# Optimization experiments

Measured on AMD Instinct MI355X. Metric: run time of the kernel, lower is better.

The kernel has to match this reference:

```python
import jax, jax.numpy as jnp
import numpy as np

HEADS = 4
DIM_HEAD = 32
DIM = 128
HIDDEN = HEADS * DIM_HEAD  # 128


def setup_inputs() -> dict:
    key = jax.random.key(0)
    k1, k2, k3 = jax.random.split(key, 3)
    B, C, H, W = 16, DIM, 128, 128
    x = jax.random.normal(k1, (B, C, H, W), dtype=jnp.float32)
    # 1x1 convs are pointwise channel mixes: weight [out_ch, in_ch]
    w_qkv = jax.random.normal(k2, (3 * HIDDEN, C), dtype=jnp.float32) * 0.05
    w_out = jax.random.normal(k3, (DIM, HIDDEN), dtype=jnp.float32) * 0.05
    b_out = jnp.zeros((DIM,), dtype=jnp.float32)
    return {"x": x, "w_qkv": w_qkv, "w_out": w_out, "b_out": b_out}


def reference(x, w_qkv, w_out, b_out):
    b, c, H, W = x.shape
    n = H * W
    scale = DIM_HEAD ** -0.5
    # to_qkv: 1x1 conv == channel GEMM -> [b, 3*hidden, n], then split (tf.split axis=1)
    qkv = jnp.einsum('oc,bchw->bohw', w_qkv, x).reshape(b, 3, HEADS, DIM_HEAD, n)
    q, k, v = qkv[:, 0], qkv[:, 1], qkv[:, 2]  # each [b, h, d, n]
    q = q * scale
    k = jax.nn.softmax(k, axis=-1)  # softmax over spatial tokens n
    context = jnp.einsum('bhdn,bhen->bhde', k, v)   # [b, h, d, e], small d x e
    out = jnp.einsum('bhde,bhdn->bhen', context, q)  # [b, h, e, n]
    out = out.reshape(b, HIDDEN, H, W)
    # to_out: 1x1 conv with bias
    return jnp.einsum('oc,bchw->bohw', w_out, out) + b_out[None, :, None, None]
```

## Files before the change

### kernel.cpp

```cpp
#include <hip/hip_runtime.h>
#include <cmath>

#define NBATCH 16
#define NCH    128
#define NPIX   16384
#define NSLOT  32

#define WS_S_OFF 0
#define WS_A_OFF (NBATCH * NSLOT * 128)
#define WS_TOT_FLOATS (WS_A_OFF + NBATCH * NSLOT * 4096)
#define WS_MBF_BYTE ((size_t)WS_TOT_FLOATS * 4)

typedef __bf16 bf16x8 __attribute__((ext_vector_type(8)));
typedef __bf16 bf16x4 __attribute__((ext_vector_type(4)));
typedef __bf16 bf16x2 __attribute__((ext_vector_type(2)));
typedef float  f32x4  __attribute__((ext_vector_type(4)));

#define MFMA16(a, b, c) __builtin_amdgcn_mfma_f32_16x16x32_bf16((a), (b), (c), 0, 0, 0)

__device__ __forceinline__ void barrier_lds() {
    asm volatile("s_waitcnt lgkmcnt(0)\n\ts_barrier" ::: "memory");
}

__global__ __launch_bounds__(256, 2) void k1_partials(const float* __restrict__ x,
                                                      const float* __restrict__ w_qkv,
                                                      float* __restrict__ ws)
{
    const int b = blockIdx.y;
    const int g = blockIdx.x;
    const int t = threadIdx.x;
    const int w = t >> 6;
    const int l = t & 63;
    const int lm = l & 15;
    const int q  = l >> 4;

    __shared__ __align__(16) __bf16 Xs[64][136];
    __shared__ __align__(16) __bf16 Ee[4][32][20][2];
    __shared__ __align__(16) __bf16 Vv[4][32][20][2];

    const float* wkv = w_qkv + 128 * NCH;
    bf16x8 wfrag[4][4];
#pragma unroll
    for (int rt = 0; rt < 4; ++rt) {
        const int row = (rt < 2) ? (w * 32 + rt * 16 + lm)
                                 : (128 + w * 32 + (rt - 2) * 16 + lm);
#pragma unroll
        for (int ks = 0; ks < 4; ++ks) {
            const float* src = wkv + row * NCH + ks * 32 + q * 8;
            float4 p0 = *(const float4*)src;
            float4 p1 = *(const float4*)(src + 4);
            bf16x8 f;
            f[0] = (__bf16)p0.x; f[1] = (__bf16)p0.y; f[2] = (__bf16)p0.z; f[3] = (__bf16)p0.w;
            f[4] = (__bf16)p1.x; f[5] = (__bf16)p1.y; f[6] = (__bf16)p1.z; f[7] = (__bf16)p1.w;
            wfrag[rt][ks] = f;
        }
    }

    f32x4 a_acc[2][2];
#pragma unroll
    for (int dt = 0; dt < 2; ++dt)
#pragma unroll
        for (int et = 0; et < 2; ++et) a_acc[dt][et] = (f32x4)0.f;
    float s8[8];
#pragma unroll
    for (int j = 0; j < 8; ++j) s8[j] = 0.f;

    float fx[8][4];
    const float* xbase = x + (size_t)(b * NCH + w * 32) * NPIX + l;

    {
        const int n0 = g * 64;
#pragma unroll
        for (int rq = 0; rq < 8; ++rq) {
            const float* xb = xbase + (size_t)(rq * 4) * NPIX + n0;
            fx[rq][0] = xb[0];
            fx[rq][1] = xb[NPIX];
            fx[rq][2] = xb[2 * NPIX];
            fx[rq][3] = xb[3 * NPIX];
        }
    }

    for (int ci = 0; ci < 8; ++ci) {
#pragma unroll
        for (int rq = 0; rq < 8; ++rq) {
            bf16x4 pk;
            pk[0] = (__bf16)fx[rq][0]; pk[1] = (__bf16)fx[rq][1];
            pk[2] = (__bf16)fx[rq][2]; pk[3] = (__bf16)fx[rq][3];
            *(bf16x4*)&Xs[l][w * 32 + rq * 4] = pk;
        }
        if (ci < 7) {
            const int n0 = (g + (ci + 1) * 32) * 64;
#pragma unroll
            for (int rq = 0; rq < 8; ++rq) {
                const float* xb = xbase + (size_t)(rq * 4) * NPIX + n0;
                fx[rq][0] = xb[0];
                fx[rq][1] = xb[NPIX];
                fx[rq][2] = xb[2 * NPIX];
                fx[rq][3] = xb[3 * NPIX];
            }
        }
        barrier_lds();

        f32x4 acc[4][4];
#pragma unroll
        for (int rt = 0; rt < 4; ++rt)
#pragma unroll
            for (int ct = 0; ct < 4; ++ct) acc[rt][ct] = (f32x4)0.f;

#pragma unroll
        for (int ks = 0; ks < 4; ++ks) {
            bf16x8 bf[4];
#pragma unroll
            for (int ct = 0; ct < 4; ++ct)
                bf[ct] = *(const bf16x8*)&Xs[ct * 16 + lm][ks * 32 + q * 8];
#pragma unroll
            for (int rt = 0; rt < 4; ++rt)
#pragma unroll
                for (int ct = 0; ct < 4; ++ct)
                    acc[rt][ct] = MFMA16(wfrag[rt][ks], bf[ct], acc[rt][ct]);
        }

#pragma unroll
        for (int hf = 0; hf < 2; ++hf) {
#pragma unroll
            for (int rt = 0; rt < 2; ++rt) {
                f32x4 v0 = acc[rt][hf * 2 + 0];
                f32x4 v1 = acc[rt][hf * 2 + 1];
#pragma unroll
                for (int r = 0; r < 4; ++r) {
                    float e0 = __expf(v0[r]);
                    float e1 = __expf(v1[r]);
                    s8[rt * 4 + r] += e0 + e1;
                    bf16x2 pw; pw[0] = (__bf16)e0; pw[1] = (__bf16)e1;
                    *(bf16x2*)&Ee[w][rt * 16 + q * 4 + r][lm][0] = pw;
                }
            }
#pragma unroll
            for (int rt = 0; rt < 2; ++rt) {
                f32x4 v0 = acc[rt + 2][hf * 2 + 0];
                f32x4 v1 = acc[rt + 2][hf * 2 + 1];
#pragma unroll
                for (int r = 0; r < 4; ++r) {
                    bf16x2 pw; pw[0] = (__bf16)v0[r]; pw[1] = (__bf16)v1[r];
                    *(bf16x2*)&Vv[w][rt * 16 + q * 4 + r][lm][0] = pw;
                }
            }
            {
                bf16x8 ea[2], vb[2];
#pragma unroll
                for (int dt = 0; dt < 2; ++dt)
                    ea[dt] = *(const bf16x8*)&Ee[w][dt * 16 + lm][q * 4][0];
#pragma unroll
                for (int et = 0; et < 2; ++et)
                    vb[et] = *(const bf16x8*)&Vv[w][et * 16 + lm][q * 4][0];
#pragma unroll
                for (int dt = 0; dt < 2; ++dt)
#pragma unroll
                    for (int et = 0; et < 2; ++et)
                        a_acc[dt][et] = MFMA16(ea[dt], vb[et], a_acc[dt][et]);
            }
        }
        barrier_lds();
    }

#pragma unroll
    for (int j = 0; j < 8; ++j) {
        float v = s8[j];
        v += __shfl_xor(v, 1);
        v += __shfl_xor(v, 2);
        v += __shfl_xor(v, 4);
        v += __shfl_xor(v, 8);
        s8[j] = v;
    }
    if (lm == 0) {
        float* Sp = ws + WS_S_OFF + (size_t)(b * NSLOT + g) * 128;
#pragma unroll
        for (int rt2 = 0; rt2 < 2; ++rt2)
#pragma unroll
            for (int r = 0; r < 4; ++r)
                Sp[w * 32 + rt2 * 16 + q * 4 + r] = s8[rt2 * 4 + r];
    }
    {
        float* Ab = ws + WS_A_OFF + (size_t)((b * NSLOT + g) * 4 + w) * 1024;
#pragma unroll
        for (int dt = 0; dt < 2; ++dt)
#pragma unroll
            for (int et = 0; et < 2; ++et)
#pragma unroll
                for (int r = 0; r < 4; ++r)
                    Ab[(dt * 16 + q * 4 + r) * 32 + et * 16 + lm] = a_acc[dt][et][r];
    }
}

__global__ __launch_bounds__(256) void k2_mprime(const float* __restrict__ w_qkv,
                                                 const float* __restrict__ w_out,
                                                 const float* __restrict__ ws,
                                                 __bf16* __restrict__ Mbf)
{
    const int b  = blockIdx.x;
    const int o0 = blockIdx.y * 32;
    const int t  = threadIdx.x;

    __shared__ float ctx[4][32][32];
    __shared__ float Ts[32][128];
    __shared__ float Wqs[32][128];
    __shared__ float Ss[128];

    if (t < 128) {
        float s = 0.f;
#pragma unroll
        for (int r = 0; r < NSLOT; ++r)
            s += ws[WS_S_OFF + (size_t)(b * NSLOT + r) * 128 + t];
        Ss[t] = s;
    }
    __syncthreads();

    for (int i = t; i < 4096; i += 256) {
        float a = 0.f;
#pragma unroll
        for (int r = 0; r < NSLOT; ++r)
            a += ws[WS_A_OFF + (size_t)(b * NSLOT + r) * 4096 + i];
        const int hh = i >> 10, d = (i >> 5) & 31, e = i & 31;
        ctx[hh][d][e] = a / Ss[hh * 32 + d];
    }
    __syncthreads();

    {
        const int oo  = t >> 3;
        const int o   = o0 + oo;
        const int hd0 = (t & 7) * 16;
        const int hh  = hd0 >> 5;
        const int db  = hd0 & 31;
        float wo[32];
#pragma unroll
        for (int e4 = 0; e4 < 32; e4 += 4)
            *(float4*)&wo[e4] = *(const float4*)&w_out[o * NCH + hh * 32 + e4];
#pragma unroll
        for (int k = 0; k < 16; ++k) {
            const int d = db + k;
            float s = 0.f;
#pragma unroll
            for (int e = 0; e < 32; ++e) s = fmaf(wo[e], ctx[hh][d][e], s);
            Ts[oo][hd0 + k] = s;
        }
    }
    __syncthreads();

    float macc[16];
#pragma unroll
    for (int ii = 0; ii < 16; ++ii) macc[ii] = 0.f;

    for (int slab = 0; slab < 4; ++slab) {
        for (int i = t; i < 32 * 128; i += 256)
            Wqs[i >> 7][i & 127] = w_qkv[(size_t)(slab * 32 + (i >> 7)) * NCH + (i & 127)];
        __syncthreads();
#pragma unroll
        for (int ii = 0; ii < 16; ++ii) {
            const int i  = t + ii * 256;
            const int oo = i >> 7;
            const int c  = i & 127;
            float s = macc[ii];
#pragma unroll
            for (int k = 0; k < 32; ++k)
                s = fmaf(Ts[oo][slab * 32 + k], Wqs[k][c], s);
            macc[ii] = s;
        }
        __syncthreads();
    }

    const float scale = 0.17677669529663687f;
#pragma unroll
    for (int ii = 0; ii < 16; ++ii) {
        const int i  = t + ii * 256;
        const int oo = i >> 7;
        const int c  = i & 127;
        Mbf[(size_t)(b * NCH + o0 + oo) * NCH + c] = (__bf16)(macc[ii] * scale);
    }
}

__global__ __launch_bounds__(256, 4) void k3_out(const float* __restrict__ x,
                                                 const float* __restrict__ bias,
                                                 const __bf16* __restrict__ Mbf,
                                                 float* __restrict__ y)
{
    const int b  = blockIdx.y;
    const int n0 = blockIdx.x * 64;
    const int t  = threadIdx.x;
    const int w  = t >> 6, l = t & 63;
    const int lm = l & 15, q = l >> 4;

    __shared__ __align__(16) __bf16 Xs[64][136];

    const __bf16* Mb = Mbf + (size_t)b * NCH * NCH;
    bf16x8 mfrag[2][4];
#pragma unroll
    for (int rt = 0; rt < 2; ++rt)
#pragma unroll
        for (int ks = 0; ks < 4; ++ks)
            mfrag[rt][ks] = *(const bf16x8*)&Mb[(size_t)(w * 32 + rt * 16 + lm) * NCH + ks * 32 + q * 8];

#pragma unroll
    for (int rq = 0; rq < 8; ++rq) {
        const int r0 = w * 32 + rq * 4;
        const float* xb = x + (size_t)(b * NCH + r0) * NPIX + n0 + l;
        float f0 = xb[0], f1 = xb[NPIX], f2 = xb[2 * NPIX], f3 = xb[3 * NPIX];
        bf16x4 pk;
        pk[0] = (__bf16)f0; pk[1] = (__bf16)f1; pk[2] = (__bf16)f2; pk[3] = (__bf16)f3;
        *(bf16x4*)&Xs[l][r0] = pk;
    }
    __syncthreads();

    f32x4 acc[2][4];
#pragma unroll
    for (int rt = 0; rt < 2; ++rt)
#pragma unroll
        for (int ct = 0; ct < 4; ++ct) acc[rt][ct] = (f32x4)0.f;

#pragma unroll
    for (int ks = 0; ks < 4; ++ks) {
        bf16x8 bf[4];
#pragma unroll
        for (int ct = 0; ct < 4; ++ct)
            bf[ct] = *(const bf16x8*)&Xs[ct * 16 + lm][ks * 32 + q * 8];
#pragma unroll
        for (int rt = 0; rt < 2; ++rt)
#pragma unroll
            for (int ct = 0; ct < 4; ++ct)
                acc[rt][ct] = MFMA16(mfrag[rt][ks], bf[ct], acc[rt][ct]);
    }

#pragma unroll
    for (int rt = 0; rt < 2; ++rt) {
#pragma unroll
        for (int r = 0; r < 4; ++r) {
            const int row = w * 32 + rt * 16 + q * 4 + r;
            const float bb = bias[row];
            float* yp = y + (size_t)(b * NCH + row) * NPIX + n0 + lm;
#pragma unroll
            for (int ct = 0; ct < 4; ++ct)
                yp[ct * 16] = acc[rt][ct][r] + bb;
        }
    }
}

extern "C" void kernel_launch(void* const* d_in, const int* in_sizes, int n_in,
                              void* d_out, int out_size, void* d_ws, size_t ws_size,
                              hipStream_t stream) {
    (void)in_sizes; (void)n_in; (void)out_size; (void)ws_size;
    const float* x     = (const float*)d_in[0];
    const float* w_qkv = (const float*)d_in[1];
    const float* w_out = (const float*)d_in[2];
    const float* b_out = (const float*)d_in[3];
    float*  y   = (float*)d_out;
    float*  ws  = (float*)d_ws;
    __bf16* Mbf = (__bf16*)((char*)d_ws + WS_MBF_BYTE);

    k1_partials<<<dim3(NSLOT, NBATCH),     256, 0, stream>>>(x, w_qkv, ws);
    k2_mprime  <<<dim3(NBATCH, 4),         256, 0, stream>>>(w_qkv, w_out, ws, Mbf);
    k3_out     <<<dim3(NPIX / 64, NBATCH), 256, 0, stream>>>(x, b_out, Mbf, y);
}
```

Measured before the change: 326.7 us.

## Use MFMA for per-batch M matrix and double-tile output kernel with prefetch

k2 is rewritten to run one block per batch. It reduces the context with vectorized loads, builds T=w_out·ctx in bf16, and forms M=T·w_qkv with bf16 MFMA instead of scalar FMA loops through shared memory. k3 now processes two 64-pixel tiles per block and prefetches the second tile's x into registers while the first is staged. This is meant to hide global load latency and cut launch and M-fragment reload overhead. The cost is fewer blocks in k2 (16), extra bf16 rounding of the intermediate T, and higher register pressure in k3.

```diff
diff --git a/kernel.cpp b/kernel.cpp
--- a/kernel.cpp
+++ b/kernel.cpp
@@ -6,8 +6,8 @@
 #define NPIX   16384
 #define NSLOT  32
 
-#define WS_S_OFF 0
-#define WS_A_OFF (NBATCH * NSLOT * 128)
+#define WS_S_OFF   0
+#define WS_A_OFF   (NBATCH * NSLOT * 128)
 #define WS_TOT_FLOATS (WS_A_OFF + NBATCH * NSLOT * 4096)
 #define WS_MBF_BYTE ((size_t)WS_TOT_FLOATS * 4)
 
@@ -197,84 +197,102 @@
                                                  const float* __restrict__ ws,
                                                  __bf16* __restrict__ Mbf)
 {
-    const int b  = blockIdx.x;
-    const int o0 = blockIdx.y * 32;
-    const int t  = threadIdx.x;
-
-    __shared__ float ctx[4][32][32];
-    __shared__ float Ts[32][128];
-    __shared__ float Wqs[32][128];
-    __shared__ float Ss[128];
+    const int b = blockIdx.x;
+    const int t = threadIdx.x;
+    const int w = t >> 6, l = t & 63;
+    const int lm = l & 15, q = l >> 4;
+
+    __shared__ __align__(16) float  ctx[4096];
+    __shared__ float  Sinv[128];
+    __shared__ __align__(16) __bf16 T[128][136];
 
     if (t < 128) {
         float s = 0.f;
 #pragma unroll
-        for (int r = 0; r < NSLOT; ++r)
-            s += ws[WS_S_OFF + (size_t)(b * NSLOT + r) * 128 + t];
-        Ss[t] = s;
+        for (int sl = 0; sl < NSLOT; ++sl)
+            s += ws[WS_S_OFF + (size_t)(b * NSLOT + sl) * 128 + t];
+        Sinv[t] = 1.f / s;
     }
     __syncthreads();
 
-    for (int i = t; i < 4096; i += 256) {
-        float a = 0.f;
-#pragma unroll
-        for (int r = 0; r < NSLOT; ++r)
-            a += ws[WS_A_OFF + (size_t)(b * NSLOT + r) * 4096 + i];
-        const int hh = i >> 10, d = (i >> 5) & 31, e = i & 31;
-        ctx[hh][d][e] = a / Ss[hh * 32 + d];
+    for (int c4 = t; c4 < 1024; c4 += 256) {
+        f32x4 a = (f32x4)0.f;
+#pragma unroll
+        for (int sl = 0; sl < NSLOT; ++sl)
+            a += *(const f32x4*)&ws[WS_A_OFF + (size_t)(b * NSLOT + sl) * 4096 + c4 * 4];
+        const float si = Sinv[c4 >> 3];
+        *(f32x4*)&ctx[c4 * 4] = a * si;
     }
     __syncthreads();
 
     {
-        const int oo  = t >> 3;
-        const int o   = o0 + oo;
-        const int hd0 = (t & 7) * 16;
-        const int hh  = hd0 >> 5;
-        const int db  = hd0 & 31;
-        float wo[32];
-#pragma unroll
-        for (int e4 = 0; e4 < 32; e4 += 4)
-            *(float4*)&wo[e4] = *(const float4*)&w_out[o * NCH + hh * 32 + e4];
-#pragma unroll
-        for (int k = 0; k < 16; ++k) {
-            const int d = db + k;
-            float s = 0.f;
-#pragma unroll
-            for (int e = 0; e < 32; ++e) s = fmaf(wo[e], ctx[hh][d][e], s);
-            Ts[oo][hd0 + k] = s;
+        const int o    = t >> 1;
+        const int half = t & 1;
+        float wo[64];
+#pragma unroll
+        for (int e4 = 0; e4 < 64; e4 += 4)
+            *(float4*)&wo[e4] = *(const float4*)&w_out[o * NCH + half * 64 + e4];
+#pragma unroll
+        for (int j8 = 0; j8 < 8; ++j8) {
+            bf16x8 pk;
+#pragma unroll
+            for (int jj = 0; jj < 8; ++jj) {
+                const int j    = j8 * 8 + jj;
+                const int hl   = j >> 5;
+                const int drow = j & 31;
+                const float* crow = &ctx[(half * 2 + hl) * 1024 + drow * 32];
+                float s = 0.f;
+#pragma unroll
+                for (int e4 = 0; e4 < 8; ++e4) {
+                    f32x4 cv = *(const f32x4*)&crow[e4 * 4];
+                    s = fmaf(wo[hl * 32 + e4 * 4 + 0], cv[0], s);
+                    s = fmaf(wo[hl * 32 + e4 * 4 + 1], cv[1], s);
+                    s = fmaf(wo[hl * 32 + e4 * 4 + 2], cv[2], s);
+                    s = fmaf(wo[hl * 32 + e4 * 4 + 3], cv[3], s);
+                }
+                pk[jj] = (__bf16)s;
+            }
+            *(bf16x8*)&T[o][half * 64 + j8 * 8] = pk;
         }
     }
     __syncthreads();
 
-    float macc[16];
-#pragma unroll
-    for (int ii = 0; ii < 16; ++ii) macc[ii] = 0.f;
-
-    for (int slab = 0; slab < 4; ++slab) {
-        for (int i = t; i < 32 * 128; i += 256)
-            Wqs[i >> 7][i & 127] = w_qkv[(size_t)(slab * 32 + (i >> 7)) * NCH + (i & 127)];
-        __syncthreads();
-#pragma unroll
-        for (int ii = 0; ii < 16; ++ii) {
-            const int i  = t + ii * 256;
-            const int oo = i >> 7;
-            const int c  = i & 127;
-            float s = macc[ii];
-#pragma unroll
-            for (int k = 0; k < 32; ++k)
-                s = fmaf(Ts[oo][slab * 32 + k], Wqs[k][c], s);
-            macc[ii] = s;
-        }
-        __syncthreads();
-    }
-
-    const float scale = 0.17677669529663687f;
-#pragma unroll
-    for (int ii = 0; ii < 16; ++ii) {
-        const int i  = t + ii * 256;
-        const int oo = i >> 7;
-        const int c  = i & 127;
-        Mbf[(size_t)(b * NCH + o0 + oo) * NCH + c] = (__bf16)(macc[ii] * scale);
+    {
+        f32x4 acc[2][8];
+#pragma unroll
+        for (int rt = 0; rt < 2; ++rt)
+#pragma unroll
+            for (int ct = 0; ct < 8; ++ct) acc[rt][ct] = (f32x4)0.f;
+
+#pragma unroll
+        for (int ks = 0; ks < 4; ++ks) {
+            bf16x8 afr[2];
+#pragma unroll
+            for (int rt = 0; rt < 2; ++rt)
+                afr[rt] = *(const bf16x8*)&T[w * 32 + rt * 16 + lm][ks * 32 + q * 8];
+#pragma unroll
+            for (int ct = 0; ct < 8; ++ct) {
+                bf16x8 bfr;
+#pragma unroll
+                for (int j = 0; j < 8; ++j)
+                    bfr[j] = (__bf16)w_qkv[(size_t)(ks * 32 + q * 8 + j) * NCH + ct * 16 + lm];
+#pragma unroll
+                for (int rt = 0; rt < 2; ++rt)
+                    acc[rt][ct] = MFMA16(afr[rt], bfr, acc[rt][ct]);
+            }
+        }
+
+        const float scale = 0.17677669529663687f;
+        __bf16* Mb = Mbf + (size_t)b * NCH * NCH;
+#pragma unroll
+        for (int rt = 0; rt < 2; ++rt)
+#pragma unroll
+            for (int r = 0; r < 4; ++r) {
+                const int o = w * 32 + rt * 16 + q * 4 + r;
+#pragma unroll
+                for (int ct = 0; ct < 8; ++ct)
+                    Mb[(size_t)o * NCH + ct * 16 + lm] = (__bf16)(acc[rt][ct][r] * scale);
+            }
     }
 }
 
@@ -284,7 +302,6 @@
                                                  float* __restrict__ y)
 {
     const int b  = blockIdx.y;
-    const int n0 = blockIdx.x * 64;
     const int t  = threadIdx.x;
     const int w  = t >> 6, l = t & 63;
     const int lm = l & 15, q = l >> 4;
@@ -299,47 +316,80 @@
         for (int ks = 0; ks < 4; ++ks)
             mfrag[rt][ks] = *(const bf16x8*)&Mb[(size_t)(w * 32 + rt * 16 + lm) * NCH + ks * 32 + q * 8];
 
-#pragma unroll
-    for (int rq = 0; rq < 8; ++rq) {
-        const int r0 = w * 32 + rq * 4;
-        const float* xb = x + (size_t)(b * NCH + r0) * NPIX + n0 + l;
-        float f0 = xb[0], f1 = xb[NPIX], f2 = xb[2 * NPIX], f3 = xb[3 * NPIX];
-        bf16x4 pk;
-        pk[0] = (__bf16)f0; pk[1] = (__bf16)f1; pk[2] = (__bf16)f2; pk[3] = (__bf16)f3;
-        *(bf16x4*)&Xs[l][r0] = pk;
-    }
-    __syncthreads();
-
-    f32x4 acc[2][4];
+    float bbr[2][4];
 #pragma unroll
     for (int rt = 0; rt < 2; ++rt)
 #pragma unroll
-        for (int ct = 0; ct < 4; ++ct) acc[rt][ct] = (f32x4)0.f;
-
-#pragma unroll
-    for (int ks = 0; ks < 4; ++ks) {
-        bf16x8 bf[4];
-#pragma unroll
-        for (int ct = 0; ct < 4; ++ct)
-            bf[ct] = *(const bf16x8*)&Xs[ct * 16 + lm][ks * 32 + q * 8];
+        for (int r = 0; r < 4; ++r)
+            bbr[rt][r] = bias[w * 32 + rt * 16 + q * 4 + r];
+
+    const float* xb3 = x + (size_t)(b * NCH + w * 32) * NPIX + l;
+    float fx[8][4];
+    {
+        const int n0 = blockIdx.x * 128;
+#pragma unroll
+        for (int rq = 0; rq < 8; ++rq) {
+            const float* xb = xb3 + (size_t)(rq * 4) * NPIX + n0;
+            fx[rq][0] = xb[0];
+            fx[rq][1] = xb[NPIX];
+            fx[rq][2] = xb[2 * NPIX];
+            fx[rq][3] = xb[3 * NPIX];
+        }
+    }
+
+    for (int jj = 0; jj < 2; ++jj) {
+#pragma unroll
+        for (int rq = 0; rq < 8; ++rq) {
+            bf16x4 pk;
+            pk[0] = (__bf16)fx[rq][0]; pk[1] = (__bf16)fx[rq][1];
+            pk[2] = (__bf16)fx[rq][2]; pk[3] = (__bf16)fx[rq][3];
+            *(bf16x4*)&Xs[l][w * 32 + rq * 4] = pk;
+        }
+        if (jj == 0) {
+            const int n1 = blockIdx.x * 128 + 64;
+#pragma unroll
+            for (int rq = 0; rq < 8; ++rq) {
+                const float* xb = xb3 + (size_t)(rq * 4) * NPIX + n1;
+                fx[rq][0] = xb[0];
+                fx[rq][1] = xb[NPIX];
+                fx[rq][2] = xb[2 * NPIX];
+                fx[rq][3] = xb[3 * NPIX];
+            }
+        }
+        barrier_lds();
+
+        f32x4 acc[2][4];
 #pragma unroll
         for (int rt = 0; rt < 2; ++rt)
 #pragma unroll
+            for (int ct = 0; ct < 4; ++ct) acc[rt][ct] = (f32x4)0.f;
+
+#pragma unroll
+        for (int ks = 0; ks < 4; ++ks) {
+            bf16x8 bf[4];
+#pragma unroll
             for (int ct = 0; ct < 4; ++ct)
-                acc[rt][ct] = MFMA16(mfrag[rt][ks], bf[ct], acc[rt][ct]);
-    }
-
-#pragma unroll
-    for (int rt = 0; rt < 2; ++rt) {
-#pragma unroll
-        for (int r = 0; r < 4; ++r) {
-            const int row = w * 32 + rt * 16 + q * 4 + r;
-            const float bb = bias[row];
-            float* yp = y + (size_t)(b * NCH + row) * NPIX + n0 + lm;
-#pragma unroll
-            for (int ct = 0; ct < 4; ++ct)
-                yp[ct * 16] = acc[rt][ct][r] + bb;
-        }
+                bf[ct] = *(const bf16x8*)&Xs[ct * 16 + lm][ks * 32 + q * 8];
+#pragma unroll
+            for (int rt = 0; rt < 2; ++rt)
+#pragma unroll
+                for (int ct = 0; ct < 4; ++ct)
+                    acc[rt][ct] = MFMA16(mfrag[rt][ks], bf[ct], acc[rt][ct]);
+        }
+
+        const int n0 = blockIdx.x * 128 + jj * 64;
+#pragma unroll
+        for (int rt = 0; rt < 2; ++rt) {
+#pragma unroll
+            for (int r = 0; r < 4; ++r) {
+                const int row = w * 32 + rt * 16 + q * 4 + r;
+                float* yp = y + (size_t)(b * NCH + row) * NPIX + n0 + lm;
+#pragma unroll
+                for (int ct = 0; ct < 4; ++ct)
+                    yp[ct * 16] = acc[rt][ct][r] + bbr[rt][r];
+            }
+        }
+        barrier_lds();
     }
 }
 
@@ -355,7 +405,7 @@
     float*  ws  = (float*)d_ws;
     __bf16* Mbf = (__bf16*)((char*)d_ws + WS_MBF_BYTE);
 
-    k1_partials<<<dim3(NSLOT, NBATCH),     256, 0, stream>>>(x, w_qkv, ws);
-    k2_mprime  <<<dim3(NBATCH, 4),         256, 0, stream>>>(w_qkv, w_out, ws, Mbf);
-    k3_out     <<<dim3(NPIX / 64, NBATCH), 256, 0, stream>>>(x, b_out, Mbf, y);
+    k1_partials<<<dim3(NSLOT, NBATCH),      256, 0, stream>>>(x, w_qkv, ws);
+    k2_mprime  <<<dim3(NBATCH),             256, 0, stream>>>(w_qkv, w_out, ws, Mbf);
+    k3_out     <<<dim3(NPIX / 128, NBATCH), 256, 0, stream>>>(x, b_out, Mbf, y);
 }
```

After: 296.0 us. 1.1x faster.
